# Optimization experiments

Hardware: AMD Instinct MI355X
Metric: run time of the kernel (lower is better)

Reference implementation:

```python
import jax, jax.numpy as jnp
import numpy as np

DIM = 256
HEADS = 4
WIN = 256          # window_size (temporal window length)
RADIUS = 32        # local_window_radius
HEAD_DIM = DIM // HEADS
SCALE = HEAD_DIM ** -0.5
NEG_INF = -1e30    # finite stand-in for -inf; safe under fp16/bf16 masking semantics via where


def _band_mask(T, radius):
    # causal local window: row i attends to j with 0 <= i - j <= radius
    i = jnp.arange(T)[:, None]
    j = jnp.arange(T)[None, :]
    d = i - j
    return jnp.where((d >= 0) & (d <= radius), 0.0, -jnp.inf).astype(jnp.float32)


def setup_inputs() -> dict:
    key = jax.random.key(0)
    k1, k2, k3 = jax.random.split(key, 3)
    B, T, C = 16, 4096, DIM
    x = jax.random.normal(k1, (B, T, C), dtype=jnp.float32)
    Wqkv = jax.random.normal(k2, (C, 3 * C), dtype=jnp.float32) * 0.02
    Wproj = jax.random.normal(k3, (C, C), dtype=jnp.float32) * 0.02
    bproj = jnp.zeros((C,), dtype=jnp.float32)
    return {"x": x, "Wqkv": Wqkv, "Wproj": Wproj, "bproj": bproj}


def reference(x, Wqkv, Wproj, bproj):
    B_prev, T_prev, C = x.shape
    # split sequence into independent temporal windows
    xw = x.reshape(-1, WIN, C)                       # [Bw, W, C]
    Bw = xw.shape[0]
    qkv = xw @ Wqkv                                  # [Bw, W, 3C]
    qkv = qkv.reshape(Bw, WIN, 3, HEADS, HEAD_DIM)
    qkv = qkv.transpose(2, 0, 3, 1, 4)               # [3, Bw, H, W, Dh]
    q, k, v = qkv[0], qkv[1], qkv[2]
    attn = jnp.einsum('bhid,bhjd->bhij', q, k) * SCALE   # [Bw, H, W, W]
    attn = attn + _band_mask(WIN, RADIUS)[None, None]
    attn = jax.nn.softmax(attn, axis=-1)
    out = jnp.einsum('bhij,bhjd->bhid', attn, v)     # [Bw, H, W, Dh]
    out = out.transpose(0, 2, 1, 3).reshape(Bw, WIN, C)
    out = out @ Wproj + bproj
    return out.reshape(B_prev, T_prev, C)
```

## Files before the change

kernel.cpp:

```cpp
#include <hip/hip_runtime.h>
#include <hip/hip_bf16.h>

typedef unsigned short u16;
typedef __attribute__((ext_vector_type(4))) float  f32x4;
typedef __attribute__((ext_vector_type(8))) short  s16x8;
typedef __attribute__((ext_vector_type(4))) short  s16x4;
typedef __attribute__((ext_vector_type(4))) int    i32x4;
typedef __attribute__((ext_vector_type(2))) unsigned int u32x2;

#define MFMA32(a,b,c) __builtin_amdgcn_mfma_f32_16x16x32_bf16((a),(b),(c),0,0,0)

__device__ __forceinline__ short f2bf(float f) {
  unsigned u = __float_as_uint(f);
  u = (u + 0x7fffu + ((u >> 16) & 1u)) >> 16;
  return (short)u;
}
__device__ __forceinline__ unsigned packbf(float lo, float hi) {
  return (unsigned)(u16)f2bf(lo) | ((unsigned)(u16)f2bf(hi) << 16);
}
__device__ __forceinline__ unsigned cvtpk(float a, float b) {
  float2 f; f.x = a; f.y = b;
  __hip_bfloat162 h = __float22bfloat162_rn(f);
  unsigned u; __builtin_memcpy(&u, &h, 4); return u;
}


__global__ __launch_bounds__(256) void k_prep(const float* __restrict__ wqkv,
                                              const float* __restrict__ wproj,
                                              u16* __restrict__ wqkvT,
                                              u16* __restrict__ wprojT) {
  int idx = blockIdx.x * 256 + threadIdx.x;
  if (idx < 768 * 256) {
    int n = idx >> 8, kk = idx & 255;
    wqkvT[idx] = (u16)f2bf(wqkv[kk * 768 + n]);
  } else {
    int j = idx - 768 * 256;
    int n = j >> 8, kk = j & 255;
    wprojT[j] = (u16)f2bf(wproj[kk * 256 + n]);
  }
}

__global__ __launch_bounds__(512, 2) void k_qkv(const float* __restrict__ x,
                                                const u16* __restrict__ wqkvT,
                                                u16* __restrict__ qkvws,
                                                int whichStride, int nmTiles) {
  __shared__ u16 Ash[128 * 256];
  const int tid = threadIdx.x;
  const int lane = tid & 63, wid = tid >> 6;
  const int wm = wid & 1, wn = wid >> 1;
  const int c15 = lane & 15, g = lane >> 4;

  int s = blockIdx.x, m, nIdx;
  if ((nmTiles & 7) == 0) {
    int xcd = s & 7, t = s >> 3;
    int lm = t / 6; nIdx = t - lm * 6; m = xcd * (nmTiles >> 3) + lm;
  } else { m = s / 6; nIdx = s - (s / 6) * 6; }
  const size_t Mbase = (size_t)m * 128;
  const int Nbase = nIdx * 128;
  const int nw0 = Nbase + wn * 32 + c15;

  s16x8 breg[2][8];
#pragma unroll
  for (int nt = 0; nt < 2; ++nt)
#pragma unroll
    for (int kc = 0; kc < 8; ++kc)
      breg[nt][kc] = *(const s16x8*)(wqkvT + (nw0 + nt * 16) * 256 + kc * 32 + g * 8);

  {
    const int row = tid >> 2, q = tid & 3;
    const float* xp = x + (Mbase + row) * 256 + q * 4;
    const unsigned swz = ((unsigned)(row & 7)) << 4;
#pragma unroll
    for (int p = 0; p < 16; ++p) {
      f32x4 v = *(const f32x4*)(xp + p * 16);
      u32x2 pk = { cvtpk(v[0], v[1]), cvtpk(v[2], v[3]) };
      unsigned b = ((unsigned)(row * 512 + p * 32 + q * 8)) ^ swz;
      *(u32x2*)((char*)Ash + b) = pk;
    }
  }
  __syncthreads();

  f32x4 acc[4][2] = {};
#pragma unroll
  for (int kc = 0; kc < 8; ++kc) {
    s16x8 af[4];
#pragma unroll
    for (int mt = 0; mt < 4; ++mt) {
      int row = wm * 64 + mt * 16 + c15;
      unsigned b = ((unsigned)(row * 512 + kc * 64 + g * 16)) ^ (((unsigned)(row & 7)) << 4);
      af[mt] = *(const s16x8*)((const char*)Ash + b);
    }
#pragma unroll
    for (int mt = 0; mt < 4; ++mt)
#pragma unroll
      for (int nt = 0; nt < 2; ++nt)
        acc[mt][nt] = MFMA32(af[mt], breg[nt][kc], acc[mt][nt]);
  }

  __syncthreads();
  u16* Csh = Ash;
#pragma unroll
  for (int mt = 0; mt < 4; ++mt)
#pragma unroll
    for (int nt = 0; nt < 2; ++nt)
#pragma unroll
      for (int r = 0; r < 4; ++r) {
        int mm = wm * 64 + mt * 16 + g * 4 + r;
        int nn = wn * 32 + nt * 16 + c15;
        unsigned addr = (unsigned)(mm * 256 + nn * 2) ^ (((unsigned)(mm & 7)) << 4);
        *(u16*)((char*)Csh + addr) = (u16)f2bf(acc[mt][nt][r]);
      }
  __syncthreads();

#pragma unroll
  for (int i = 0; i < 4; ++i) {
    int c = tid + 512 * i;
    int mm = c >> 4;
    int n0 = (c & 15) * 8;
    unsigned addr = (unsigned)(mm * 256 + n0 * 2) ^ (((unsigned)(mm & 7)) << 4);
    i32x4 v = *(const i32x4*)((const char*)Csh + addr);
    int n = Nbase + n0;
    int which = n >> 8, h = (n >> 6) & 3, dd = n & 63;
    size_t mg = Mbase + mm;
    size_t o = (size_t)which * whichStride + (size_t)h * 16384
             + (mg >> 8) * 65536 + (mg & 255) * 64 + dd;
    *(i32x4*)(qkvws + o) = v;
  }
}

__global__ __launch_bounds__(512) void k_attn_proj(const u16* __restrict__ qws,
                                                   const u16* __restrict__ kws,
                                                   const u16* __restrict__ vws,
                                                   const u16* __restrict__ wprojT,
                                                   const float* __restrict__ bias,
                                                   float* __restrict__ out) {
  __shared__ u16 Osh[256 * 256];
  const int tid = threadIdx.x;
  const int lane = tid & 63, wid = tid >> 6;
  const int head = wid >> 1, qhalf = wid & 1;
  const int c15 = lane & 15, g = lane >> 4;
  const int win = blockIdx.x;

  const size_t hb = (size_t)(win * 4 + head) * 16384;
  const u16* Qp = qws + hb;
  const u16* Kp = kws + hb;
  const u16* Vp = vws + hb;
  const int start = qhalf * 8;

  s16x8 klo[4] = {}, khi[4] = {};
  s16x8 vfr[4][4] = {};

#define LOADKV(jt, slot) do {                                                \
    const u16* _p = Kp + (jt) * 1024 + c15 * 64 + g * 8;                     \
    klo[slot] = *(const s16x8*)_p;                                           \
    khi[slot] = *(const s16x8*)(_p + 32);                                    \
    const int _rb = (jt) * 16 + ((g & 1) << 3);                              \
    _Pragma("unroll")                                                        \
    for (int _dt = 0; _dt < 4; ++_dt) {                                      \
      s16x8 _t;                                                              \
      _Pragma("unroll")                                                      \
      for (int _i = 0; _i < 8; ++_i)                                         \
        _t[_i] = (short)Vp[(_rb + _i) * 64 + _dt * 16 + c15];                \
      vfr[slot][_dt] = _t;                                                   \
    }                                                                        \
  } while (0)

  if (start >= 2) LOADKV(start - 2, 2);
  if (start >= 1) LOADKV(start - 1, 3);
  LOADKV(start, 0);

#pragma unroll
  for (int ii = 0; ii < 8; ++ii) {
    const int i16 = start + ii;
    const int sP = (ii + 1) & 3;
    const int s0 = ii & 3;
    const int s1 = (ii + 3) & 3;
    const int s2 = (ii + 2) & 3;
    if (ii < 7) LOADKV(i16 + 1, sP);

    const u16* qp = Qp + i16 * 1024 + c15 * 64 + g * 8;
    const s16x8 qf0 = *(const s16x8*)qp;
    const s16x8 qf1 = *(const s16x8*)(qp + 32);

    f32x4 sT0 = {}, sT1 = {}, sT2 = {};
    sT0 = MFMA32(klo[s0], qf0, sT0);
    sT0 = MFMA32(khi[s0], qf1, sT0);
    if (i16 >= 1) { sT1 = MFMA32(klo[s1], qf0, sT1); sT1 = MFMA32(khi[s1], qf1, sT1); }
    if (i16 >= 2) { sT2 = MFMA32(klo[s2], qf0, sT2); sT2 = MFMA32(khi[s2], qf1, sT2); }

    const int qrow = i16 * 16 + c15;
    float e0[4], e1[4], e2[4];
    float vmax = -3.0e38f;
#pragma unroll
    for (int r = 0; r < 4; ++r) {
      int dd = qrow - (i16 * 16 + g * 4 + r);
      e0[r] = (dd >= 0 && dd <= 32) ? sT0[r] * 0.125f : -1.0e30f;
      vmax = fmaxf(vmax, e0[r]);
    }
    if (i16 >= 1) {
#pragma unroll
      for (int r = 0; r < 4; ++r) {
        e1[r] = sT1[r] * 0.125f;
        vmax = fmaxf(vmax, e1[r]);
      }
    }
    if (i16 >= 2) {
#pragma unroll
      for (int r = 0; r < 4; ++r) {
        int dd = qrow - ((i16 - 2) * 16 + g * 4 + r);
        e2[r] = (dd <= 32) ? sT2[r] * 0.125f : -1.0e30f;
        vmax = fmaxf(vmax, e2[r]);
      }
    }
    vmax = fmaxf(vmax, __shfl_xor(vmax, 16));
    vmax = fmaxf(vmax, __shfl_xor(vmax, 32));
    float ssum = 0.0f;
#pragma unroll
    for (int r = 0; r < 4; ++r) { e0[r] = __expf(e0[r] - vmax); ssum += e0[r]; }
    if (i16 >= 1) {
#pragma unroll
      for (int r = 0; r < 4; ++r) { e1[r] = __expf(e1[r] - vmax); ssum += e1[r]; }
    }
    if (i16 >= 2) {
#pragma unroll
      for (int r = 0; r < 4; ++r) { e2[r] = __expf(e2[r] - vmax); ssum += e2[r]; }
    }
    ssum += __shfl_xor(ssum, 16);
    ssum += __shfl_xor(ssum, 32);
    const float inv = 1.0f / ssum;

    unsigned c0a = packbf(e0[0] * inv, e0[1] * inv), c0b = packbf(e0[2] * inv, e0[3] * inv);
    unsigned c1a = 0, c1b = 0, c2a = 0, c2b = 0;
    if (i16 >= 1) { c1a = packbf(e1[0] * inv, e1[1] * inv); c1b = packbf(e1[2] * inv, e1[3] * inv); }
    if (i16 >= 2) { c2a = packbf(e2[0] * inv, e2[1] * inv); c2b = packbf(e2[2] * inv, e2[3] * inv); }

    const int src0 = ((g & 1) << 5) + c15;
    const int src1 = src0 + 16;
    const bool alo = (g < 2);
#define MKFRAG(pa, ua, ub) do {                                             \
      int _t0 = __shfl((int)(ua), src0), _t1 = __shfl((int)(ub), src0);     \
      int _t2 = __shfl((int)(ua), src1), _t3 = __shfl((int)(ub), src1);     \
      i32x4 _ti = { alo ? _t0 : 0, alo ? _t1 : 0, alo ? _t2 : 0, alo ? _t3 : 0 }; \
      pa = *(s16x8*)&_ti;                                                   \
    } while (0)
    s16x8 pa0, pa1, pa2;
    MKFRAG(pa0, c0a, c0b);
    MKFRAG(pa1, c1a, c1b);
    MKFRAG(pa2, c2a, c2b);
#undef MKFRAG

    f32x4 oa[4] = {};
#pragma unroll
    for (int dt = 0; dt < 4; ++dt) {
      oa[dt] = MFMA32(pa0, vfr[s0][dt], oa[dt]);
      if (i16 >= 1) oa[dt] = MFMA32(pa1, vfr[s1][dt], oa[dt]);
      if (i16 >= 2) oa[dt] = MFMA32(pa2, vfr[s2][dt], oa[dt]);
    }

#pragma unroll
    for (int dt = 0; dt < 4; ++dt) {
#pragma unroll
      for (int r = 0; r < 4; ++r) {
        int row = i16 * 16 + g * 4 + r;
        unsigned addr = (unsigned)(row * 512 + head * 128 + dt * 32 + c15 * 2);
        addr ^= ((unsigned)(row & 7)) << 4;
        *(u16*)((char*)Osh + addr) = (u16)f2bf(oa[dt][r]);
      }
    }
  }
#undef LOADKV

  __syncthreads();

  s16x8 afr[2][8];
#pragma unroll
  for (int mt = 0; mt < 2; ++mt) {
#pragma unroll
    for (int ks = 0; ks < 8; ++ks) {
      int row = wid * 32 + mt * 16 + c15;
      unsigned addr = ((unsigned)(row * 512 + ks * 64 + g * 16)) ^ (((unsigned)(row & 7)) << 4);
      afr[mt][ks] = *(const s16x8*)((const char*)Osh + addr);
    }
  }
  const int wbase = win * 256;
  for (int nt = 0; nt < 16; ++nt) {
    s16x8 bfr[8];
#pragma unroll
    for (int ks = 0; ks < 8; ++ks)
      bfr[ks] = *(const s16x8*)(wprojT + (nt * 16 + c15) * 256 + ks * 32 + g * 8);
    const float bv = bias[nt * 16 + c15];
    f32x4 a0 = {bv, bv, bv, bv};
    f32x4 a1 = {bv, bv, bv, bv};
#pragma unroll
    for (int ks = 0; ks < 8; ++ks) {
      a0 = MFMA32(afr[0][ks], bfr[ks], a0);
      a1 = MFMA32(afr[1][ks], bfr[ks], a1);
    }
    const int m0 = wbase + wid * 32;
#pragma unroll
    for (int r = 0; r < 4; ++r) {
      out[(size_t)(m0 + g * 4 + r) * 256 + nt * 16 + c15] = a0[r];
      out[(size_t)(m0 + 16 + g * 4 + r) * 256 + nt * 16 + c15] = a1[r];
    }
  }
}

extern "C" void kernel_launch(void* const* d_in, const int* in_sizes, int n_in,
                              void* d_out, int out_size, void* d_ws, size_t ws_size,
                              hipStream_t stream) {
  (void)in_sizes; (void)n_in; (void)out_size;
  const float* x     = (const float*)d_in[0];
  const float* wqkv  = (const float*)d_in[1];
  const float* wproj = (const float*)d_in[2];
  const float* bias  = (const float*)d_in[3];
  float* out = (float*)d_out;
  char* ws = (char*)d_ws;

  const size_t wBytes = (size_t)768 * 256 * 2 + (size_t)256 * 256 * 2;
  u16* wqkvT  = (u16*)ws;
  u16* wprojT = (u16*)(ws + (size_t)768 * 256 * 2);
  u16* qkvbuf = (u16*)(ws + wBytes);

  const size_t perWin = 393216;
  size_t avail = (ws_size > wBytes) ? (ws_size - wBytes) : 0;
  int cwMax = (int)(avail / perWin);
  if (cwMax < 1) return;
  if (cwMax > 256) cwMax = 256;
  if (cwMax >= 4) cwMax &= ~3;

  k_prep<<<1024, 256, 0, stream>>>(wqkv, wproj, wqkvT, wprojT);

  for (int w0 = 0; w0 < 256; w0 += cwMax) {
    int cw = 256 - w0 < cwMax ? 256 - w0 : cwMax;
    int whichStride = cw * 65536;
    int nm = cw * 2;
    k_qkv<<<nm * 6, 512, 0, stream>>>(x + (size_t)w0 * 65536, wqkvT, qkvbuf, whichStride, nm);
    k_attn_proj<<<cw, 512, 0, stream>>>(qkvbuf,
                                        qkvbuf + (size_t)whichStride,
                                        qkvbuf + (size_t)2 * whichStride,
                                        wprojT, bias,
                                        out + (size_t)w0 * 65536);
  }
}
```

Before: 124.3 us.

## Pre-convert x to swizzled bf16 and stream it into LDS via global_load_lds

Adds a k_conv pass that converts x from fp32 to bf16 once, already in the swizzled LDS layout, into a workspace buffer. k_qkv then fills shared memory with direct global-to-LDS 16-byte loads instead of reading fp32 and converting in every N-tile block. Previously each of the six N-tile blocks re-read and re-converted the same x rows. Weight fragments are now loaded per k-chunk rather than held in registers, and the occupancy hint rises from 2 to 4. The cost is an extra kernel launch plus a bf16 round trip through memory, and the workspace per window grows, so fewer windows fit per chunk.

```diff
diff --git a/kernel.cpp b/kernel.cpp
--- a/kernel.cpp
+++ b/kernel.cpp
@@ -4,9 +4,7 @@
 typedef unsigned short u16;
 typedef __attribute__((ext_vector_type(4))) float  f32x4;
 typedef __attribute__((ext_vector_type(8))) short  s16x8;
-typedef __attribute__((ext_vector_type(4))) short  s16x4;
 typedef __attribute__((ext_vector_type(4))) int    i32x4;
-typedef __attribute__((ext_vector_type(2))) unsigned int u32x2;
 
 #define MFMA32(a,b,c) __builtin_amdgcn_mfma_f32_16x16x32_bf16((a),(b),(c),0,0,0)
 
@@ -22,6 +20,11 @@
   float2 f; f.x = a; f.y = b;
   __hip_bfloat162 h = __float22bfloat162_rn(f);
   unsigned u; __builtin_memcpy(&u, &h, 4); return u;
+}
+__device__ __forceinline__ void gload_lds16(const u16* g, u16* l) {
+  __builtin_amdgcn_global_load_lds(
+      (const __attribute__((address_space(1))) void*)g,
+      (__attribute__((address_space(3))) void*)l, 16, 0, 0);
 }
 
 
@@ -40,7 +43,27 @@
   }
 }
 
-__global__ __launch_bounds__(512, 2) void k_qkv(const float* __restrict__ x,
+__global__ __launch_bounds__(512) void k_conv(const float* __restrict__ x,
+                                              u16* __restrict__ xbfs) {
+  const int tid = threadIdx.x;
+  const size_t base = (size_t)blockIdx.x * 32768;
+#pragma unroll
+  for (int p = 0; p < 8; ++p) {
+    int c = tid + 512 * p;
+    unsigned D = (unsigned)c * 16;
+    unsigned row = D >> 9;
+    unsigned vD = D ^ ((row & 7u) << 4);
+    unsigned vchunk = (vD >> 4) & 31u;
+    const float* sp = x + base + row * 256 + vchunk * 8;
+    f32x4 a = *(const f32x4*)sp;
+    f32x4 b = *(const f32x4*)(sp + 4);
+    i32x4 o = { (int)cvtpk(a[0], a[1]), (int)cvtpk(a[2], a[3]),
+                (int)cvtpk(b[0], b[1]), (int)cvtpk(b[2], b[3]) };
+    *(i32x4*)(xbfs + base + (size_t)c * 8) = o;
+  }
+}
+
+__global__ __launch_bounds__(512, 4) void k_qkv(const u16* __restrict__ xbfs,
                                                 const u16* __restrict__ wqkvT,
                                                 u16* __restrict__ qkvws,
                                                 int whichStride, int nmTiles) {
@@ -55,28 +78,15 @@
     int xcd = s & 7, t = s >> 3;
     int lm = t / 6; nIdx = t - lm * 6; m = xcd * (nmTiles >> 3) + lm;
   } else { m = s / 6; nIdx = s - (s / 6) * 6; }
-  const size_t Mbase = (size_t)m * 128;
   const int Nbase = nIdx * 128;
   const int nw0 = Nbase + wn * 32 + c15;
 
-  s16x8 breg[2][8];
-#pragma unroll
-  for (int nt = 0; nt < 2; ++nt)
-#pragma unroll
-    for (int kc = 0; kc < 8; ++kc)
-      breg[nt][kc] = *(const s16x8*)(wqkvT + (nw0 + nt * 16) * 256 + kc * 32 + g * 8);
-
   {
-    const int row = tid >> 2, q = tid & 3;
-    const float* xp = x + (Mbase + row) * 256 + q * 4;
-    const unsigned swz = ((unsigned)(row & 7)) << 4;
-#pragma unroll
-    for (int p = 0; p < 16; ++p) {
-      f32x4 v = *(const f32x4*)(xp + p * 16);
-      u32x2 pk = { cvtpk(v[0], v[1]), cvtpk(v[2], v[3]) };
-      unsigned b = ((unsigned)(row * 512 + p * 32 + q * 8)) ^ swz;
-      *(u32x2*)((char*)Ash + b) = pk;
-    }
+    const u16* src = xbfs + (size_t)m * 32768 + wid * 4096 + lane * 8;
+    u16* dst = Ash + wid * 4096;
+#pragma unroll
+    for (int p = 0; p < 8; ++p)
+      gload_lds16(src + p * 512, dst + p * 512);
   }
   __syncthreads();
 
@@ -90,11 +100,13 @@
       unsigned b = ((unsigned)(row * 512 + kc * 64 + g * 16)) ^ (((unsigned)(row & 7)) << 4);
       af[mt] = *(const s16x8*)((const char*)Ash + b);
     }
-#pragma unroll
-    for (int mt = 0; mt < 4; ++mt)
-#pragma unroll
-      for (int nt = 0; nt < 2; ++nt)
-        acc[mt][nt] = MFMA32(af[mt], breg[nt][kc], acc[mt][nt]);
+    s16x8 b0 = *(const s16x8*)(wqkvT + nw0 * 256 + kc * 32 + g * 8);
+    s16x8 b1 = *(const s16x8*)(wqkvT + (nw0 + 16) * 256 + kc * 32 + g * 8);
+#pragma unroll
+    for (int mt = 0; mt < 4; ++mt) {
+      acc[mt][0] = MFMA32(af[mt], b0, acc[mt][0]);
+      acc[mt][1] = MFMA32(af[mt], b1, acc[mt][1]);
+    }
   }
 
   __syncthreads();
@@ -121,7 +133,7 @@
     i32x4 v = *(const i32x4*)((const char*)Csh + addr);
     int n = Nbase + n0;
     int which = n >> 8, h = (n >> 6) & 3, dd = n & 63;
-    size_t mg = Mbase + mm;
+    size_t mg = (size_t)m * 128 + mm;
     size_t o = (size_t)which * whichStride + (size_t)h * 16384
              + (mg >> 8) * 65536 + (mg & 255) * 64 + dd;
     *(i32x4*)(qkvws + o) = v;
@@ -321,12 +333,13 @@
   u16* wprojT = (u16*)(ws + (size_t)768 * 256 * 2);
   u16* qkvbuf = (u16*)(ws + wBytes);
 
-  const size_t perWin = 393216;
+  const size_t perWin = 393216 + 131072;
   size_t avail = (ws_size > wBytes) ? (ws_size - wBytes) : 0;
   int cwMax = (int)(avail / perWin);
   if (cwMax < 1) return;
   if (cwMax > 256) cwMax = 256;
   if (cwMax >= 4) cwMax &= ~3;
+  u16* xbfs = qkvbuf + (size_t)cwMax * 3 * 65536;
 
   k_prep<<<1024, 256, 0, stream>>>(wqkv, wproj, wqkvT, wprojT);
 
@@ -334,7 +347,8 @@
     int cw = 256 - w0 < cwMax ? 256 - w0 : cwMax;
     int whichStride = cw * 65536;
     int nm = cw * 2;
-    k_qkv<<<nm * 6, 512, 0, stream>>>(x + (size_t)w0 * 65536, wqkvT, qkvbuf, whichStride, nm);
+    k_conv<<<nm, 512, 0, stream>>>(x + (size_t)w0 * 65536, xbfs);
+    k_qkv<<<nm * 6, 512, 0, stream>>>(xbfs, wqkvT, qkvbuf, whichStride, nm);
     k_attn_proj<<<cw, 512, 0, stream>>>(qkvbuf,
                                         qkvbuf + (size_t)whichStride,
                                         qkvbuf + (size_t)2 * whichStride,
```

After: 143.4 us. 15.3% more time.
